# Kernel tuning notes

Hardware: AMD Instinct MI355X
Metric: run time of the kernel (lower is better)

The kernel has to match this reference:

```python
import jax, jax.numpy as jnp
import numpy as np

BATCH = 16384
DIM = 1024
NUM_LAYERS = 4


def setup_inputs() -> dict:
    key = jax.random.key(0)
    k_x, k_w, k_b = jax.random.split(key, 3)
    x0 = jax.random.normal(k_x, (BATCH, DIM), dtype=jnp.float32)
    # torch.rand -> uniform [0,1)
    W = jax.random.uniform(k_w, (NUM_LAYERS, DIM), dtype=jnp.float32)
    b = jax.random.uniform(k_b, (NUM_LAYERS, DIM), dtype=jnp.float32)
    return {"x0": x0, "W": W, "b": b}


def reference(x0, W, b):
    # Cross layer: bmm(x0[:, :, None], xl[:, None, :]) @ W == x0 * (xl @ W)
    # (scalar per batch row), mathematically identical without the O(B*d^2)
    # intermediate.
    xl = x0
    for l in range(NUM_LAYERS):
        s = jnp.einsum('bd,d->b', xl, W[l])  # [B]
        xl = x0 * s[:, None] + b[l] + xl
    return xl
```

## Files before the change

kernel.cpp:

```cpp
#include <hip/hip_runtime.h>

#define BATCH   16384
#define DIM     1024
#define NLAYERS 4
#define NF4     (DIM / 4)
#define THREADS 256
#define NBLOCKS 2048

__global__ __launch_bounds__(THREADS) void crossnet_kernel(
    const float* __restrict__ x0,
    const float* __restrict__ W,
    const float* __restrict__ b,
    float* __restrict__ out)
{
    __shared__ float4 lW[NLAYERS * NF4];
    __shared__ float4 lBsum[NF4];
    __shared__ float  redc[3][4];

    const int tid  = threadIdx.x;
    const int lane = tid & 63;
    const int wv   = tid >> 6;

    const float4* Wv = reinterpret_cast<const float4*>(W);
    const float4* bv = reinterpret_cast<const float4*>(b);

#pragma unroll
    for (int i = 0; i < NLAYERS * NF4 / THREADS; ++i)
        lW[tid + i * THREADS] = Wv[tid + i * THREADS];

    float4 b0 = bv[0 * NF4 + tid];
    float4 b1 = bv[1 * NF4 + tid];
    float4 b2 = bv[2 * NF4 + tid];
    float4 b3 = bv[3 * NF4 + tid];
    float4 w1 = Wv[1 * NF4 + tid];
    float4 w2 = Wv[2 * NF4 + tid];
    float4 w3 = Wv[3 * NF4 + tid];

    float4 pre = b0;
    float c1 = pre.x * w1.x + pre.y * w1.y + pre.z * w1.z + pre.w * w1.w;
    pre.x += b1.x; pre.y += b1.y; pre.z += b1.z; pre.w += b1.w;
    float c2 = pre.x * w2.x + pre.y * w2.y + pre.z * w2.z + pre.w * w2.w;
    pre.x += b2.x; pre.y += b2.y; pre.z += b2.z; pre.w += b2.w;
    float c3 = pre.x * w3.x + pre.y * w3.y + pre.z * w3.z + pre.w * w3.w;
    pre.x += b3.x; pre.y += b3.y; pre.z += b3.z; pre.w += b3.w;
    lBsum[tid] = pre;

#pragma unroll
    for (int off = 32; off; off >>= 1) {
        c1 += __shfl_xor(c1, off, 64);
        c2 += __shfl_xor(c2, off, 64);
        c3 += __shfl_xor(c3, off, 64);
    }
    if (lane == 0) { redc[0][wv] = c1; redc[1][wv] = c2; redc[2][wv] = c3; }
    __syncthreads();
    const float cp1 = redc[0][0] + redc[0][1] + redc[0][2] + redc[0][3];
    const float cp2 = redc[1][0] + redc[1][1] + redc[1][2] + redc[1][3];
    const float cp3 = redc[2][0] + redc[2][1] + redc[2][2] + redc[2][3];

    float4 bs[4];
#pragma unroll
    for (int j = 0; j < 4; ++j) bs[j] = lBsum[j * 64 + lane];

    const int gw = blockIdx.x * (THREADS / 64) + wv;
    const int nw = NBLOCKS * (THREADS / 64);

    for (int row = gw; row < BATCH; row += nw) {
        const float4* xv = reinterpret_cast<const float4*>(x0) + (size_t)row * NF4;
        float4 x[4];
#pragma unroll
        for (int j = 0; j < 4; ++j) x[j] = xv[j * 64 + lane];

        float d0 = 0.f, d1 = 0.f, d2 = 0.f, d3 = 0.f;
#pragma unroll
        for (int j = 0; j < 4; ++j) {
            const int fi = j * 64 + lane;
            float4 a0 = lW[0 * NF4 + fi];
            float4 a1 = lW[1 * NF4 + fi];
            float4 a2 = lW[2 * NF4 + fi];
            float4 a3 = lW[3 * NF4 + fi];
            d0 += x[j].x * a0.x + x[j].y * a0.y + x[j].z * a0.z + x[j].w * a0.w;
            d1 += x[j].x * a1.x + x[j].y * a1.y + x[j].z * a1.z + x[j].w * a1.w;
            d2 += x[j].x * a2.x + x[j].y * a2.y + x[j].z * a2.z + x[j].w * a2.w;
            d3 += x[j].x * a3.x + x[j].y * a3.y + x[j].z * a3.z + x[j].w * a3.w;
        }
#pragma unroll
        for (int off = 32; off; off >>= 1) {
            d0 += __shfl_xor(d0, off, 64);
            d1 += __shfl_xor(d1, off, 64);
            d2 += __shfl_xor(d2, off, 64);
            d3 += __shfl_xor(d3, off, 64);
        }

        float alpha = 1.0f;
        float s0 = alpha * d0;              alpha += s0;
        float s1 = fmaf(alpha, d1, cp1);    alpha += s1;
        float s2 = fmaf(alpha, d2, cp2);    alpha += s2;
        float s3 = fmaf(alpha, d3, cp3);    alpha += s3;

        float4* ov = reinterpret_cast<float4*>(out) + (size_t)row * NF4;
#pragma unroll
        for (int j = 0; j < 4; ++j) {
            float4 o;
            o.x = fmaf(alpha, x[j].x, bs[j].x);
            o.y = fmaf(alpha, x[j].y, bs[j].y);
            o.z = fmaf(alpha, x[j].z, bs[j].z);
            o.w = fmaf(alpha, x[j].w, bs[j].w);
            ov[j * 64 + lane] = o;
        }
    }
}

extern "C" void kernel_launch(void* const* d_in, const int* in_sizes, int n_in,
                              void* d_out, int out_size, void* d_ws, size_t ws_size,
                              hipStream_t stream) {
    const float* x0 = (const float*)d_in[0];
    const float* W  = (const float*)d_in[1];
    const float* b  = (const float*)d_in[2];
    float* out      = (float*)d_out;

    crossnet_kernel<<<NBLOCKS, THREADS, 0, stream>>>(x0, W, b, out);
}
```

Baseline: 26.31 us.

## Assign fixed row chunks per wave with triple-buffered prefetch and nontemporal stores

Cuts the grid to 512 blocks and gives each wave a contiguous chunk of 8 rows. Row loads are software-pipelined with a 3-slot register buffer, and the first two rows are issued before the W/b preamble so that setup overlaps with memory latency. Output is written with nontemporal stores so it does not pollute the cache. In exchange the kernel uses more registers and has fewer blocks, which may lower occupancy, and the LDS scratch reuse adds extra barriers.

```diff
diff --git a/kernel.cpp b/kernel.cpp
--- a/kernel.cpp
+++ b/kernel.cpp
@@ -5,7 +5,10 @@
 #define NLAYERS 4
 #define NF4     (DIM / 4)
 #define THREADS 256
-#define NBLOCKS 2048
+#define NBLOCKS 512
+#define ROWS    8
+
+typedef float floatx4 __attribute__((ext_vector_type(4)));
 
 __global__ __launch_bounds__(THREADS) void crossnet_kernel(
     const float* __restrict__ x0,
@@ -15,11 +18,22 @@
 {
     __shared__ float4 lW[NLAYERS * NF4];
     __shared__ float4 lBsum[NF4];
-    __shared__ float  redc[3][4];
 
     const int tid  = threadIdx.x;
     const int lane = tid & 63;
     const int wv   = tid >> 6;
+
+    const int    gw   = blockIdx.x * (THREADS / 64) + wv;
+    const size_t base = (size_t)gw * ROWS;
+
+    const float4* xbase = reinterpret_cast<const float4*>(x0) + base * NF4 + lane;
+    floatx4*      obase = reinterpret_cast<floatx4*>(out)     + base * NF4 + lane;
+
+    float4 X[3][4];
+#pragma unroll
+    for (int j = 0; j < 4; ++j) X[0][j] = xbase[0 * NF4 + j * 64];
+#pragma unroll
+    for (int j = 0; j < 4; ++j) X[1][j] = xbase[1 * NF4 + j * 64];
 
     const float4* Wv = reinterpret_cast<const float4*>(W);
     const float4* bv = reinterpret_cast<const float4*>(b);
@@ -43,7 +57,6 @@
     pre.x += b2.x; pre.y += b2.y; pre.z += b2.z; pre.w += b2.w;
     float c3 = pre.x * w3.x + pre.y * w3.y + pre.z * w3.z + pre.w * w3.w;
     pre.x += b3.x; pre.y += b3.y; pre.z += b3.z; pre.w += b3.w;
-    lBsum[tid] = pre;
 
 #pragma unroll
     for (int off = 32; off; off >>= 1) {
@@ -51,37 +64,41 @@
         c2 += __shfl_xor(c2, off, 64);
         c3 += __shfl_xor(c3, off, 64);
     }
-    if (lane == 0) { redc[0][wv] = c1; redc[1][wv] = c2; redc[2][wv] = c3; }
+    float* scratch = reinterpret_cast<float*>(lBsum);
+    if (lane == 0) { scratch[wv] = c1; scratch[4 + wv] = c2; scratch[8 + wv] = c3; }
     __syncthreads();
-    const float cp1 = redc[0][0] + redc[0][1] + redc[0][2] + redc[0][3];
-    const float cp2 = redc[1][0] + redc[1][1] + redc[1][2] + redc[1][3];
-    const float cp3 = redc[2][0] + redc[2][1] + redc[2][2] + redc[2][3];
+    const float cp1 = scratch[0] + scratch[1] + scratch[2]  + scratch[3];
+    const float cp2 = scratch[4] + scratch[5] + scratch[6]  + scratch[7];
+    const float cp3 = scratch[8] + scratch[9] + scratch[10] + scratch[11];
+    __syncthreads();
+    lBsum[tid] = pre;
+    __syncthreads();
 
     float4 bs[4];
 #pragma unroll
     for (int j = 0; j < 4; ++j) bs[j] = lBsum[j * 64 + lane];
 
-    const int gw = blockIdx.x * (THREADS / 64) + wv;
-    const int nw = NBLOCKS * (THREADS / 64);
-
-    for (int row = gw; row < BATCH; row += nw) {
-        const float4* xv = reinterpret_cast<const float4*>(x0) + (size_t)row * NF4;
-        float4 x[4];
 #pragma unroll
-        for (int j = 0; j < 4; ++j) x[j] = xv[j * 64 + lane];
+    for (int k = 0; k < ROWS; ++k) {
+        if (k + 2 < ROWS) {
+#pragma unroll
+            for (int j = 0; j < 4; ++j)
+                X[(k + 2) % 3][j] = xbase[(size_t)(k + 2) * NF4 + j * 64];
+        }
 
         float d0 = 0.f, d1 = 0.f, d2 = 0.f, d3 = 0.f;
 #pragma unroll
         for (int j = 0; j < 4; ++j) {
             const int fi = j * 64 + lane;
-            float4 a0 = lW[0 * NF4 + fi];
-            float4 a1 = lW[1 * NF4 + fi];
-            float4 a2 = lW[2 * NF4 + fi];
-            float4 a3 = lW[3 * NF4 + fi];
-            d0 += x[j].x * a0.x + x[j].y * a0.y + x[j].z * a0.z + x[j].w * a0.w;
-            d1 += x[j].x * a1.x + x[j].y * a1.y + x[j].z * a1.z + x[j].w * a1.w;
-            d2 += x[j].x * a2.x + x[j].y * a2.y + x[j].z * a2.z + x[j].w * a2.w;
-            d3 += x[j].x * a3.x + x[j].y * a3.y + x[j].z * a3.z + x[j].w * a3.w;
+            const float4 xx = X[k % 3][j];
+            const float4 a0 = lW[0 * NF4 + fi];
+            const float4 a1 = lW[1 * NF4 + fi];
+            const float4 a2 = lW[2 * NF4 + fi];
+            const float4 a3 = lW[3 * NF4 + fi];
+            d0 += xx.x * a0.x + xx.y * a0.y + xx.z * a0.z + xx.w * a0.w;
+            d1 += xx.x * a1.x + xx.y * a1.y + xx.z * a1.z + xx.w * a1.w;
+            d2 += xx.x * a2.x + xx.y * a2.y + xx.z * a2.z + xx.w * a2.w;
+            d3 += xx.x * a3.x + xx.y * a3.y + xx.z * a3.z + xx.w * a3.w;
         }
 #pragma unroll
         for (int off = 32; off; off >>= 1) {
@@ -91,21 +108,21 @@
             d3 += __shfl_xor(d3, off, 64);
         }
 
-        float alpha = 1.0f;
-        float s0 = alpha * d0;              alpha += s0;
-        float s1 = fmaf(alpha, d1, cp1);    alpha += s1;
-        float s2 = fmaf(alpha, d2, cp2);    alpha += s2;
-        float s3 = fmaf(alpha, d3, cp3);    alpha += s3;
+        float al = 1.0f;
+        { float s = al * d0;            al += s;
+          s = fmaf(al, d1, cp1);        al += s;
+          s = fmaf(al, d2, cp2);        al += s;
+          s = fmaf(al, d3, cp3);        al += s; }
 
-        float4* ov = reinterpret_cast<float4*>(out) + (size_t)row * NF4;
 #pragma unroll
         for (int j = 0; j < 4; ++j) {
-            float4 o;
-            o.x = fmaf(alpha, x[j].x, bs[j].x);
-            o.y = fmaf(alpha, x[j].y, bs[j].y);
-            o.z = fmaf(alpha, x[j].z, bs[j].z);
-            o.w = fmaf(alpha, x[j].w, bs[j].w);
-            ov[j * 64 + lane] = o;
+            const float4 xx = X[k % 3][j];
+            floatx4 o;
+            o.x = fmaf(al, xx.x, bs[j].x);
+            o.y = fmaf(al, xx.y, bs[j].y);
+            o.z = fmaf(al, xx.z, bs[j].z);
+            o.w = fmaf(al, xx.w, bs[j].w);
+            __builtin_nontemporal_store(o, &obase[(size_t)k * NF4 + j * 64]);
         }
     }
 }
```

Measured after the change: 30.49 us. 15.9% more time.
